# Performance work log

Measured on AMD Instinct MI355X. Metric: run time of the kernel, lower is better.

The kernel has to match this reference:

```python
import jax, jax.numpy as jnp
import numpy as np

N_NODES = 100000
N_EDGES = 1600000
B = 256
H = 512
HEADS = 8
DH = H // HEADS


def setup_inputs() -> dict:
    key = jax.random.key(0)
    ks = list(jax.random.split(key, 24))
    def nrm(i, shape, s=0.02):
        return jax.random.normal(ks[i], shape, jnp.float32) * s
    inp = {}
    inp["text_features"] = jax.random.normal(ks[0], (B, 768), jnp.float32)
    inp["video_features"] = jax.random.normal(ks[1], (B, 512), jnp.float32)
    inp["x"] = jax.random.normal(ks[2], (N_NODES, 64), jnp.float32)
    inp["edge_index"] = jax.random.randint(ks[3], (2, N_EDGES), 0, N_NODES, dtype=jnp.int32)
    # sorted node->graph assignment covering all B graphs (no empty segments)
    inp["batch_idx"] = ((jnp.arange(N_NODES) * B) // N_NODES).astype(jnp.int32)
    inp["Wt"] = nrm(4, (768, H)); inp["bt"] = jnp.zeros((H,), jnp.float32)
    inp["Wv"] = nrm(5, (512, H)); inp["bv"] = jnp.zeros((H,), jnp.float32)
    inp["Wq"] = nrm(6, (H, H)); inp["bq"] = jnp.zeros((H,), jnp.float32)
    inp["Wk"] = nrm(7, (H, H)); inp["bk"] = jnp.zeros((H,), jnp.float32)
    inp["Wva"] = nrm(8, (H, H)); inp["bva"] = jnp.zeros((H,), jnp.float32)
    inp["Wo"] = nrm(9, (H, H)); inp["bo"] = jnp.zeros((H,), jnp.float32)
    inp["Wf"] = nrm(10, (2 * H, H)); inp["bf"] = jnp.zeros((H,), jnp.float32)
    inp["G1W"] = nrm(11, (64, 128)); inp["G1b"] = jnp.zeros((128,), jnp.float32)
    inp["G2W"] = nrm(12, (128, 128)); inp["G2b"] = jnp.zeros((128,), jnp.float32)
    inp["G3W"] = nrm(13, (128, 256)); inp["G3b"] = jnp.zeros((256,), jnp.float32)
    inp["Wff"] = nrm(14, (H + 256, H)); inp["bff"] = jnp.zeros((H,), jnp.float32)
    inp["Wb"] = nrm(15, (H, 2)); inp["bb"] = jnp.zeros((2,), jnp.float32)
    inp["Wa"] = nrm(16, (H, 2)); inp["ba"] = jnp.zeros((2,), jnp.float32)
    return inp


def _gcn_conv(h, W, b, src, dst, dis):
    # PyG GCNConv: linear transform, symmetric-normalized aggregation w/ self-loops, bias
    hw = h @ W                                       # [N, C]
    norm = dis[src] * dis[dst]                       # [E]
    msg = hw[src] * norm[:, None]                    # [E, C]
    agg = jax.ops.segment_sum(msg, dst, num_segments=h.shape[0])
    agg = agg + hw * (dis * dis)[:, None]            # self-loop messages
    return agg + b


def reference(text_features, video_features, x, edge_index, batch_idx, Wt, bt, Wv, bv, Wq, bq, Wk, bk, Wva, bva, Wo, bo, Wf, bf, G1W, G1b, G2W, G2b, G3W, G3b, Wff, bff, Wb, bb, Wa, ba):
    # encoders (dropout is eval-mode no-op)
    text_enc = jax.nn.relu(text_features @ Wt + bt)      # [B, H]
    video_enc = jax.nn.relu(video_features @ Wv + bv)    # [B, H]
    # multihead attention; torch seq lens are both 1 (batch acts as N)
    q = (text_enc @ Wq + bq).reshape(B, HEADS, 1, DH)
    k = (video_enc @ Wk + bk).reshape(B, HEADS, 1, DH)
    v = (video_enc @ Wva + bva).reshape(B, HEADS, 1, DH)
    scores = jnp.einsum('bhqd,bhkd->bhqk', q, k) / np.float32(np.sqrt(DH))
    w = jax.nn.softmax(scores, axis=-1)
    attn = jnp.einsum('bhqk,bhkd->bhqd', w, v).reshape(B, H)
    text_attended = attn @ Wo + bo
    # multimodal fusion
    fused = jax.nn.relu(jnp.concatenate([text_attended, video_enc], axis=1) @ Wf + bf)
    # GCN stack
    src, dst = edge_index[0], edge_index[1]
    deg = jax.ops.segment_sum(jnp.ones((N_EDGES,), jnp.float32), dst, num_segments=N_NODES) + 1.0
    dis = jax.lax.rsqrt(deg)
    h = jax.nn.elu(_gcn_conv(x, G1W, G1b, src, dst, dis))
    h = jax.nn.elu(_gcn_conv(h, G2W, G2b, src, dst, dis))
    h = _gcn_conv(h, G3W, G3b, src, dst, dis)            # [N, 256]
    # per-graph mean pooling (the original per-batch Python loop, as one segment-mean)
    counts = jax.ops.segment_sum(jnp.ones((N_NODES,), jnp.float32), batch_idx, num_segments=B)
    pooled = jax.ops.segment_sum(h, batch_idx, num_segments=B) / counts[:, None]  # [B, 256]
    # final fusion + classifier heads
    final = jax.nn.relu(jnp.concatenate([fused, pooled], axis=1) @ Wff + bff)
    bullying = jax.nn.log_softmax(final @ Wb + bb, axis=1)
    aggression = jax.nn.log_softmax(final @ Wa + ba, axis=1)
    return bullying, aggression
```

## Files before the change

kernel.cpp:

```cpp
#include <hip/hip_runtime.h>
#include <hip/hip_bf16.h>

#define N_NODES 100000
#define NPAD    100096
#define N_EDGES 1600000
#define BATCH   256
#define HDIM    512

typedef unsigned short u16;
typedef __attribute__((ext_vector_type(8))) short bf16x8;
typedef __attribute__((ext_vector_type(8))) unsigned short u16x8;
typedef __attribute__((ext_vector_type(4))) float f32x4;

__device__ __forceinline__ float bf2f(u16 u) {
    union { unsigned i; float f; } v; v.i = ((unsigned)u) << 16; return v.f;
}
__device__ __forceinline__ u16 f2bf(float f) {
    __hip_bfloat16 h = __float2bfloat16(f);
    return *reinterpret_cast<u16*>(&h);
}

template<int K, int ACT, int SCALE>
__global__ __launch_bounds__(256) void gemm_mfma(
        const u16* __restrict__ A, const u16* __restrict__ Wt,
        const float* __restrict__ bias, const float* __restrict__ dis,
        u16* __restrict__ C, int N) {
    constexpr int RB = K * 2;
    __shared__ u16 As[128 * K];
    __shared__ u16 Bs[128 * K];
    const int tid  = threadIdx.x;
    const int lane = tid & 63;
    const int w    = tid >> 6;
    const int wr   = w >> 1, wc = w & 1;
    const int row0 = blockIdx.y * 128;
    const int col0 = blockIdx.x * 128;

    constexpr int WB     = 128 * RB / 4;
    constexpr int PASSES = WB / 1024;
    const size_t Abase = (size_t)row0 * K;
    const size_t Bbase = (size_t)col0 * K;
    #pragma unroll
    for (int p = 0; p < PASSES; ++p) {
        int Lb  = w * WB + p * 1024;
        int L   = Lb + lane * 16;
        int row = L / RB;
        int cb  = L % RB;
        int scb = cb ^ ((row & 7) << 4);
        const u16* ga = A  + Abase + (size_t)row * K + (scb >> 1);
        const u16* gb = Wt + Bbase + (size_t)row * K + (scb >> 1);
        __builtin_amdgcn_global_load_lds((const __attribute__((address_space(1))) void*)ga,
            (__attribute__((address_space(3))) void*)&As[Lb >> 1], 16, 0, 0);
        __builtin_amdgcn_global_load_lds((const __attribute__((address_space(1))) void*)gb,
            (__attribute__((address_space(3))) void*)&Bs[Lb >> 1], 16, 0, 0);
    }
    asm volatile("s_waitcnt vmcnt(0)" ::: "memory");
    __syncthreads();

    const int rl = lane & 15;
    const int kg = lane >> 4;
    f32x4 acc[4][4] = {};
    #pragma unroll
    for (int s = 0; s < K / 32; ++s) {
        bf16x8 af[4], bg[4];
        #pragma unroll
        for (int m = 0; m < 4; ++m) {
            int row = wr * 64 + m * 16 + rl;
            int cb  = s * 64 + kg * 16;
            int scb = cb ^ ((row & 7) << 4);
            af[m] = *(const bf16x8*)&As[(row * RB + scb) >> 1];
        }
        #pragma unroll
        for (int n = 0; n < 4; ++n) {
            int row = wc * 64 + n * 16 + rl;
            int cb  = s * 64 + kg * 16;
            int scb = cb ^ ((row & 7) << 4);
            bg[n] = *(const bf16x8*)&Bs[(row * RB + scb) >> 1];
        }
        #pragma unroll
        for (int m = 0; m < 4; ++m)
            #pragma unroll
            for (int n = 0; n < 4; ++n)
                acc[m][n] = __builtin_amdgcn_mfma_f32_16x16x32_bf16(af[m], bg[n], acc[m][n], 0, 0, 0);
    }

    #pragma unroll
    for (int m = 0; m < 4; ++m) {
        #pragma unroll
        for (int r = 0; r < 4; ++r) {
            int grow = row0 + wr * 64 + m * 16 + kg * 4 + r;
            float ds = SCALE ? dis[grow] : 1.f;
            #pragma unroll
            for (int n = 0; n < 4; ++n) {
                int gcol = col0 + wc * 64 + n * 16 + rl;
                float v = acc[m][n][r] + bias[gcol];
                if (ACT == 2) v = v > 0.f ? v : expm1f(v);
                C[(size_t)grow * N + gcol] = f2bf(v * ds);
            }
        }
    }
}

template<int ACT>
__global__ __launch_bounds__(256) void gemm64(
        const u16* __restrict__ A, const u16* __restrict__ Wt,
        const float* __restrict__ bias, u16* __restrict__ C,
        int K, int lda, int ldc) {
    __shared__ u16 As[64 * 64];
    __shared__ u16 Bs[64 * 64];
    const int tid  = threadIdx.x;
    const int lane = tid & 63;
    const int w    = tid >> 6;
    const int wr   = w >> 1, wc = w & 1;
    const int row0 = blockIdx.y * 64;
    const int col0 = blockIdx.x * 64;
    const int rl = lane & 15;
    const int kg = lane >> 4;
    f32x4 acc[2][2] = {};

    for (int k0 = 0; k0 < K; k0 += 64) {
        #pragma unroll
        for (int p = 0; p < 2; ++p) {
            int Lb  = w * 2048 + p * 1024;
            int L   = Lb + lane * 16;
            int row = L >> 7;
            int cb  = L & 127;
            int scb = cb ^ ((row & 7) << 4);
            const u16* ga = A  + (size_t)(row0 + row) * lda + k0 + (scb >> 1);
            const u16* gb = Wt + (size_t)(col0 + row) * K   + k0 + (scb >> 1);
            __builtin_amdgcn_global_load_lds((const __attribute__((address_space(1))) void*)ga,
                (__attribute__((address_space(3))) void*)&As[Lb >> 1], 16, 0, 0);
            __builtin_amdgcn_global_load_lds((const __attribute__((address_space(1))) void*)gb,
                (__attribute__((address_space(3))) void*)&Bs[Lb >> 1], 16, 0, 0);
        }
        asm volatile("s_waitcnt vmcnt(0)" ::: "memory");
        __syncthreads();
        #pragma unroll
        for (int s = 0; s < 2; ++s) {
            bf16x8 af[2], bg[2];
            #pragma unroll
            for (int m = 0; m < 2; ++m) {
                int row = wr * 32 + m * 16 + rl;
                int cb  = s * 64 + kg * 16;
                int scb = cb ^ ((row & 7) << 4);
                af[m] = *(const bf16x8*)&As[(row * 128 + scb) >> 1];
            }
            #pragma unroll
            for (int n = 0; n < 2; ++n) {
                int row = wc * 32 + n * 16 + rl;
                int cb  = s * 64 + kg * 16;
                int scb = cb ^ ((row & 7) << 4);
                bg[n] = *(const bf16x8*)&Bs[(row * 128 + scb) >> 1];
            }
            #pragma unroll
            for (int m = 0; m < 2; ++m)
                #pragma unroll
                for (int n = 0; n < 2; ++n)
                    acc[m][n] = __builtin_amdgcn_mfma_f32_16x16x32_bf16(af[m], bg[n], acc[m][n], 0, 0, 0);
        }
        __syncthreads();
    }

    #pragma unroll
    for (int m = 0; m < 2; ++m) {
        #pragma unroll
        for (int r = 0; r < 4; ++r) {
            int grow = row0 + wr * 32 + m * 16 + kg * 4 + r;
            #pragma unroll
            for (int n = 0; n < 2; ++n) {
                int gcol = col0 + wc * 32 + n * 16 + rl;
                float v = acc[m][n][r] + bias[gcol];
                if (ACT == 1) v = fmaxf(v, 0.f);
                C[(size_t)grow * ldc + gcol] = f2bf(v);
            }
        }
    }
}

template<int K, int N>
__device__ __forceinline__ void tw(const float* __restrict__ W, u16* __restrict__ Wt, int t) {
    int n = t / K, k = t - n * K;
    Wt[t] = f2bf(W[(size_t)k * N + n]);
}

#define DEG_BLKS 6250

__global__ void prep_deg(const int* __restrict__ dstE, int* __restrict__ deg,
                         int* __restrict__ slot,
                         const float* __restrict__ G1W, u16* __restrict__ g1wt,
                         const float* __restrict__ G2W, u16* __restrict__ g2wt,
                         const float* __restrict__ Wv,  u16* __restrict__ WvT,
                         const float* __restrict__ Wva, u16* __restrict__ WvaT,
                         const float* __restrict__ Wo,  u16* __restrict__ WoT,
                         const float* __restrict__ Wf,  u16* __restrict__ WfT,
                         const float* __restrict__ video, u16* __restrict__ vidbf) {
    int bid = blockIdx.x;
    const int tid = threadIdx.x;
    if (bid < DEG_BLKS) {
        int e = bid * 256 + tid;
        slot[e] = atomicAdd(&deg[dstE[e]], 1);
        return;
    }
    bid -= DEG_BLKS;
    if (bid < 32)        { tw<64, 128>  (G1W, g1wt, bid * 256 + tid); }
    else if (bid < 96)   { tw<128, 128> (G2W, g2wt, (bid - 32) * 256 + tid); }
    else if (bid < 1120) { tw<512, 512> (Wv,  WvT,  (bid - 96) * 256 + tid); }
    else if (bid < 2144) { tw<512, 512> (Wva, WvaT, (bid - 1120) * 256 + tid); }
    else if (bid < 3168) { tw<512, 512> (Wo,  WoT,  (bid - 2144) * 256 + tid); }
    else if (bid < 5216) { tw<1024, 512>(Wf,  WfT,  (bid - 3168) * 256 + tid); }
    else { int t = (bid - 5216) * 256 + tid; vidbf[t] = f2bf(video[t]); }
}

__global__ void final_fused(const u16* __restrict__ fusedb,
                            const float* __restrict__ pooled, const float* __restrict__ counts,
                            const float* __restrict__ G3W, const float* __restrict__ G3b,
                            const float* __restrict__ Wff, const float* __restrict__ bff,
                            const float* __restrict__ Wb,  const float* __restrict__ bb,
                            const float* __restrict__ Wa,  const float* __restrict__ ba,
                            float* __restrict__ out) {
    __shared__ float cat[768], fin[512], pp[128];
    __shared__ float rd[4][4];
    const int b = blockIdx.x, tid = threadIdx.x;
    cat[tid] = bf2f(fusedb[b * 512 + tid]);
    cat[tid + 256] = bf2f(fusedb[b * 512 + 256 + tid]);
    float inv = 1.f / counts[b];
    if (tid < 128) pp[tid] = pooled[b * 128 + tid] * inv;
    __syncthreads();
    {
        float s = G3b[tid];
        #pragma unroll 8
        for (int k = 0; k < 128; ++k) s += pp[k] * G3W[k * 256 + tid];
        cat[512 + tid] = s;
    }
    __syncthreads();
    {
        float a0 = bff[tid], a1 = bff[tid + 256];
        #pragma unroll 8
        for (int k = 0; k < 768; ++k) {
            float xv = cat[k];
            a0 += xv * Wff[k * 512 + tid];
            a1 += xv * Wff[k * 512 + tid + 256];
        }
        fin[tid] = fmaxf(a0, 0.f);
        fin[tid + 256] = fmaxf(a1, 0.f);
    }
    __syncthreads();
    float z0 = 0.f, z1 = 0.f, y0 = 0.f, y1 = 0.f;
    for (int k = tid; k < 512; k += 256) {
        float f = fin[k];
        z0 += f * Wb[2 * k];
        z1 += f * Wb[2 * k + 1];
        y0 += f * Wa[2 * k];
        y1 += f * Wa[2 * k + 1];
    }
    #pragma unroll
    for (int off = 32; off > 0; off >>= 1) {
        z0 += __shfl_down(z0, off);
        z1 += __shfl_down(z1, off);
        y0 += __shfl_down(y0, off);
        y1 += __shfl_down(y1, off);
    }
    int ww = tid >> 6;
    if ((tid & 63) == 0) { rd[ww][0] = z0; rd[ww][1] = z1; rd[ww][2] = y0; rd[ww][3] = y1; }
    __syncthreads();
    if (tid == 0) {
        float Z0 = rd[0][0] + rd[1][0] + rd[2][0] + rd[3][0] + bb[0];
        float Z1 = rd[0][1] + rd[1][1] + rd[2][1] + rd[3][1] + bb[1];
        float Y0 = rd[0][2] + rd[1][2] + rd[2][2] + rd[3][2] + ba[0];
        float Y1 = rd[0][3] + rd[1][3] + rd[2][3] + rd[3][3] + ba[1];
        float m = fmaxf(Z0, Z1);
        float l = m + logf(expf(Z0 - m) + expf(Z1 - m));
        out[b * 2 + 0] = Z0 - l;
        out[b * 2 + 1] = Z1 - l;
        float m2 = fmaxf(Y0, Y1);
        float l2 = m2 + logf(expf(Y0 - m2) + expf(Y1 - m2));
        out[512 + b * 2 + 0] = Y0 - l2;
        out[512 + b * 2 + 1] = Y1 - l2;
    }
}

__global__ void scan1(const int* __restrict__ in, int* __restrict__ out,
                      int* __restrict__ bsum, float* __restrict__ dis, int n) {
    __shared__ int ts[256];
    const int tid = threadIdx.x;
    const int base = blockIdx.x * 1024;
    int v[4];
    #pragma unroll
    for (int i = 0; i < 4; ++i) {
        int idx = base + tid * 4 + i;
        v[i] = (idx < n) ? in[idx] : 0;
        if (idx < NPAD) dis[idx] = rsqrtf((float)v[i] + 1.f);
    }
    ts[tid] = v[0] + v[1] + v[2] + v[3];
    __syncthreads();
    for (int off = 1; off < 256; off <<= 1) {
        int val = (tid >= off) ? ts[tid - off] : 0;
        __syncthreads();
        ts[tid] += val;
        __syncthreads();
    }
    int run = (tid == 0) ? 0 : ts[tid - 1];
    if (tid == 255) bsum[blockIdx.x] = ts[255];
    #pragma unroll
    for (int i = 0; i < 4; ++i) {
        int idx = base + tid * 4 + i;
        if (idx < n) out[idx] = run;
        run += v[i];
    }
}

__global__ void scan2(int* __restrict__ bsum, int nb) {
    int l = threadIdx.x;
    int a = (l < nb) ? bsum[l] : 0;
    int b = (l + 64 < nb) ? bsum[l + 64] : 0;
    int oa = a, ob = b;
    #pragma unroll
    for (int off = 1; off < 64; off <<= 1) {
        int t = __shfl_up(a, off);
        if (l >= off) a += t;
    }
    int totA = __shfl(a, 63);
    #pragma unroll
    for (int off = 1; off < 64; off <<= 1) {
        int t = __shfl_up(b, off);
        if (l >= off) b += t;
    }
    if (l < nb) bsum[l] = a - oa;
    if (l + 64 < nb) bsum[l + 64] = totA + b - ob;
}

__global__ void csr_scatter3(const int* __restrict__ srcE, const int* __restrict__ dstE,
                             const int* __restrict__ partial, const int* __restrict__ bsum,
                             const int* __restrict__ slot,
                             int* __restrict__ csr_src, int* __restrict__ rowptr) {
    int e = blockIdx.x * blockDim.x + threadIdx.x;
    if (e <= N_NODES) rowptr[e] = (e < N_NODES) ? (partial[e] + bsum[e >> 10]) : N_EDGES;
    if (e < N_EDGES) {
        int d = dstE[e];
        csr_src[partial[d] + bsum[d >> 10] + slot[e]] = srcE[e];
    }
}

__global__ void scale_rows64_bf16(const float* __restrict__ x, const float* __restrict__ dis,
                                  u16* __restrict__ out) {
    int t = blockIdx.x * blockDim.x + threadIdx.x;
    if (t >= N_NODES * 64) return;
    out[t] = f2bf(x[t] * dis[t >> 6]);
}

template<int C>
__global__ void csr_agg_bf16(const u16* __restrict__ Hs, const int* __restrict__ rowptr,
                             const int* __restrict__ csr_src, const float* __restrict__ dis,
                             u16* __restrict__ out) {
    constexpr int LPG = C / 8;
    constexpr int G   = 64 / LPG;
    int node = blockIdx.x * 4 + (threadIdx.x >> 6);
    if (node >= N_NODES) return;
    int lane = threadIdx.x & 63;
    int g  = lane / LPG;
    int cl = lane % LPG;
    int s0 = rowptr[node], s1 = rowptr[node + 1];
    float a[8] = {};
    if (g == 0) {
        u16x8 v = *(const u16x8*)&Hs[(size_t)node * C + cl * 8];
        #pragma unroll
        for (int j = 0; j < 8; ++j) a[j] = bf2f(v[j]);
    }
    int e = s0 + g;
    while (e + 3 * G < s1) {
        int sA = csr_src[e], sB = csr_src[e + G];
        int sC = csr_src[e + 2 * G], sD = csr_src[e + 3 * G];
        u16x8 vA = *(const u16x8*)&Hs[(size_t)sA * C + cl * 8];
        u16x8 vB = *(const u16x8*)&Hs[(size_t)sB * C + cl * 8];
        u16x8 vC = *(const u16x8*)&Hs[(size_t)sC * C + cl * 8];
        u16x8 vD = *(const u16x8*)&Hs[(size_t)sD * C + cl * 8];
        #pragma unroll
        for (int j = 0; j < 8; ++j)
            a[j] += (bf2f(vA[j]) + bf2f(vB[j])) + (bf2f(vC[j]) + bf2f(vD[j]));
        e += 4 * G;
    }
    while (e < s1) {
        int s = csr_src[e];
        u16x8 v = *(const u16x8*)&Hs[(size_t)s * C + cl * 8];
        #pragma unroll
        for (int j = 0; j < 8; ++j) a[j] += bf2f(v[j]);
        e += G;
    }
    #pragma unroll
    for (int m = LPG; m < 64; m <<= 1)
        #pragma unroll
        for (int j = 0; j < 8; ++j) a[j] += __shfl_xor(a[j], m);
    if (g == 0) {
        float dd = dis[node];
        u16x8 o;
        #pragma unroll
        for (int j = 0; j < 8; ++j) o[j] = f2bf(a[j] * dd);
        *(u16x8*)&out[(size_t)node * C + cl * 8] = o;
    }
}

__global__ __launch_bounds__(256) void csr_agg_pool(
        const u16* __restrict__ Hs, const int* __restrict__ rowptr,
        const int* __restrict__ csr_src, const float* __restrict__ dis,
        const int* __restrict__ batch,
        float* __restrict__ pooled, float* __restrict__ counts) {
    __shared__ float bins[2][128];
    __shared__ int cnt[2];
    const int tid = threadIdx.x;
    const int base = blockIdx.x * 16;
    if (tid < 128) { bins[0][tid] = 0.f; bins[1][tid] = 0.f; }
    if (tid < 2) cnt[tid] = 0;
    __syncthreads();
    const int lane = tid & 63;
    const int w = tid >> 6;
    const int g = lane >> 4;
    const int cl = lane & 15;
    const int b0 = batch[base];
    #pragma unroll
    for (int i = 0; i < 4; ++i) {
        const int node = base + w * 4 + i;
        const int s0 = rowptr[node], s1 = rowptr[node + 1];
        float a[8] = {};
        if (g == 0) {
            u16x8 v = *(const u16x8*)&Hs[(size_t)node * 128 + cl * 8];
            #pragma unroll
            for (int j = 0; j < 8; ++j) a[j] = bf2f(v[j]);
        }
        int e = s0 + g;
        while (e + 12 < s1) {
            int sA = csr_src[e], sB = csr_src[e + 4];
            int sC = csr_src[e + 8], sD = csr_src[e + 12];
            u16x8 vA = *(const u16x8*)&Hs[(size_t)sA * 128 + cl * 8];
            u16x8 vB = *(const u16x8*)&Hs[(size_t)sB * 128 + cl * 8];
            u16x8 vC = *(const u16x8*)&Hs[(size_t)sC * 128 + cl * 8];
            u16x8 vD = *(const u16x8*)&Hs[(size_t)sD * 128 + cl * 8];
            #pragma unroll
            for (int j = 0; j < 8; ++j)
                a[j] += (bf2f(vA[j]) + bf2f(vB[j])) + (bf2f(vC[j]) + bf2f(vD[j]));
            e += 16;
        }
        while (e < s1) {
            int s = csr_src[e];
            u16x8 v = *(const u16x8*)&Hs[(size_t)s * 128 + cl * 8];
            #pragma unroll
            for (int j = 0; j < 8; ++j) a[j] += bf2f(v[j]);
            e += 4;
        }
        #pragma unroll
        for (int m = 16; m < 64; m <<= 1)
            #pragma unroll
            for (int j = 0; j < 8; ++j) a[j] += __shfl_xor(a[j], m);
        if (g == 0) {
            int bin = (batch[node] != b0) ? 1 : 0;
            float dd = dis[node];
            #pragma unroll
            for (int j = 0; j < 8; ++j) atomicAdd(&bins[bin][cl * 8 + j], a[j] * dd);
            if (cl == 0) atomicAdd(&cnt[bin], 1);
        }
    }
    __syncthreads();
    int bin = tid >> 7, c = tid & 127;
    if (cnt[bin] > 0) atomicAdd(&pooled[(b0 + bin) * 128 + c], bins[bin][c]);
    if (tid < 2 && cnt[tid] > 0) atomicAdd(&counts[b0 + tid], (float)cnt[tid]);
}

extern "C" void kernel_launch(void* const* d_in, const int* in_sizes, int n_in,
                              void* d_out, int out_size, void* d_ws, size_t ws_size,
                              hipStream_t stream) {
    const float* video = (const float*)d_in[1];
    const float* x     = (const float*)d_in[2];
    const int*   eidx  = (const int*)d_in[3];
    const int*   batch = (const int*)d_in[4];
    const float* Wv  = (const float*)d_in[7],  *bv  = (const float*)d_in[8];
    const float* Wva = (const float*)d_in[13], *bva = (const float*)d_in[14];
    const float* Wo  = (const float*)d_in[15], *bo  = (const float*)d_in[16];
    const float* Wf  = (const float*)d_in[17], *bf  = (const float*)d_in[18];
    const float* G1W = (const float*)d_in[19], *G1b = (const float*)d_in[20];
    const float* G2W = (const float*)d_in[21], *G2b = (const float*)d_in[22];
    const float* G3W = (const float*)d_in[23], *G3b = (const float*)d_in[24];
    const float* Wff = (const float*)d_in[25], *bff = (const float*)d_in[26];
    const float* Wb  = (const float*)d_in[27], *bb  = (const float*)d_in[28];
    const float* Wa  = (const float*)d_in[29], *ba  = (const float*)d_in[30];
    const int* srcE = eidx;
    const int* dstE = eidx + N_EDGES;

    char* wsc = (char*)d_ws;
    size_t off = 0;
    auto alloc = [&](size_t bytes) { char* p = wsc + off; off += (bytes + 255) & ~(size_t)255; return p; };
    u16*   bufA    = (u16*)  alloc((size_t)NPAD * 128 * 2);
    u16*   bufB    = (u16*)  alloc((size_t)NPAD * 128 * 2);
    float* dis     = (float*)alloc(NPAD * 4);
    int*   deg     = (int*)  alloc(NPAD * 4);
    int*   partial = (int*)  alloc(N_NODES * 4);
    int*   rowptr  = (int*)  alloc((N_NODES + 1) * 4);
    int*   slot    = (int*)  alloc((size_t)N_EDGES * 4);
    int*   csrsrc  = (int*)  alloc((size_t)N_EDGES * 4);
    int*   bsum    = (int*)  alloc(128 * 4);
    u16*   g1wt    = (u16*)  alloc(128 * 64 * 2);
    u16*   g2wt    = (u16*)  alloc(128 * 128 * 2);
    u16*   WvT     = (u16*)  alloc(512 * 512 * 2);
    u16*   WvaT    = (u16*)  alloc(512 * 512 * 2);
    u16*   WoT     = (u16*)  alloc(512 * 512 * 2);
    u16*   WfT     = (u16*)  alloc(512 * 1024 * 2);
    u16*   vidbf   = (u16*)  alloc(BATCH * 512 * 2);
    u16*   catb    = (u16*)  alloc(BATCH * 1024 * 2);
    u16*   vattnb  = (u16*)  alloc(BATCH * 512 * 2);
    u16*   fusedb  = (u16*)  alloc(BATCH * 512 * 2);
    float* pooled  = (float*)alloc((BATCH * 128 + BATCH) * 4);
    float* counts  = pooled + BATCH * 128;

    const int NB = (N_NODES + 1023) / 1024;

    hipMemsetAsync(deg, 0, NPAD * 4, stream);
    hipMemsetAsync(pooled, 0, (BATCH * 128 + BATCH) * 4, stream);
    prep_deg<<<DEG_BLKS + 5728, 256, 0, stream>>>(dstE, deg, slot,
        G1W, g1wt, G2W, g2wt, Wv, WvT, Wva, WvaT, Wo, WoT, Wf, WfT, video, vidbf);

    scan1<<<NB, 256, 0, stream>>>(deg, partial, bsum, dis, N_NODES);
    scan2<<<1, 64, 0, stream>>>(bsum, NB);
    csr_scatter3<<<(N_EDGES + 255) / 256, 256, 0, stream>>>(srcE, dstE, partial, bsum,
                                                            slot, csrsrc, rowptr);

    dim3 fe512(8, 4);
    gemm64<1><<<fe512, 256, 0, stream>>>(vidbf, WvT, bv, catb + 512, 512, 512, 1024);
    gemm64<0><<<fe512, 256, 0, stream>>>(catb + 512, WvaT, bva, vattnb, 512, 1024, 512);
    gemm64<0><<<fe512, 256, 0, stream>>>(vattnb, WoT, bo, catb, 512, 512, 1024);
    gemm64<1><<<fe512, 256, 0, stream>>>(catb, WfT, bf, fusedb, 1024, 1024, 512);

    scale_rows64_bf16<<<(N_NODES * 64 + 255) / 256, 256, 0, stream>>>(x, dis, bufA);
    csr_agg_bf16<64><<<(N_NODES + 3) / 4, 256, 0, stream>>>(bufA, rowptr, csrsrc, dis, bufB);
    gemm_mfma<64, 2, 1><<<dim3(1, NPAD / 128), 256, 0, stream>>>(bufB, g1wt, G1b, dis, bufA, 128);
    csr_agg_bf16<128><<<(N_NODES + 3) / 4, 256, 0, stream>>>(bufA, rowptr, csrsrc, dis, bufB);
    gemm_mfma<128, 2, 1><<<dim3(1, NPAD / 128), 256, 0, stream>>>(bufB, g2wt, G2b, dis, bufA, 128);
    csr_agg_pool<<<N_NODES / 16, 256, 0, stream>>>(bufA, rowptr, csrsrc, dis, batch, pooled, counts);

    final_fused<<<BATCH, 256, 0, stream>>>(fusedb, pooled, counts, G3W, G3b,
                                           Wff, bff, Wb, bb, Wa, ba, (float*)d_out);
}
```

Baseline: 448.0 us.

## Store GCN hidden features in fp8 for gather aggregation; fuse scatter with scaling

The two 128-wide GEMM outputs are now written as fp8 e4m3 instead of bf16. The two aggregation kernels that follow gather these fp8 rows, which halves the bytes per random neighbor read in the memory-bound edge gathers. The CSR scatter and the x-scaling kernel are merged into one launch, and the two memsets are combined into one by making the pooled buffer contiguous with deg. The risk is accuracy: e4m3 keeps only 3 mantissa bits for the hidden activations, which may exceed tolerance.

Measured after the change: 434.1 us. -3.1%, faster.

```diff
diff --git a/kernel.cpp b/kernel.cpp
--- a/kernel.cpp
+++ b/kernel.cpp
@@ -1,5 +1,6 @@
 #include <hip/hip_runtime.h>
 #include <hip/hip_bf16.h>
+#include <hip/hip_fp8.h>
 
 #define N_NODES 100000
 #define NPAD    100096
@@ -8,8 +9,10 @@
 #define HDIM    512
 
 typedef unsigned short u16;
+typedef unsigned char  u8;
 typedef __attribute__((ext_vector_type(8))) short bf16x8;
 typedef __attribute__((ext_vector_type(8))) unsigned short u16x8;
+typedef __attribute__((ext_vector_type(8))) unsigned char u8x8;
 typedef __attribute__((ext_vector_type(4))) float f32x4;
 
 __device__ __forceinline__ float bf2f(u16 u) {
@@ -19,12 +22,18 @@
     __hip_bfloat16 h = __float2bfloat16(f);
     return *reinterpret_cast<u16*>(&h);
 }
-
-template<int K, int ACT, int SCALE>
+__device__ __forceinline__ u8 f2fp8(float f) {
+    __hip_fp8_e4m3 q(f); return (u8)q.__x;
+}
+__device__ __forceinline__ float fp82f(u8 b) {
+    __hip_fp8_e4m3 q; q.__x = (__hip_fp8_storage_t)b; return (float)q;
+}
+
+template<int K, int ACT, int SCALE, int F8>
 __global__ __launch_bounds__(256) void gemm_mfma(
         const u16* __restrict__ A, const u16* __restrict__ Wt,
         const float* __restrict__ bias, const float* __restrict__ dis,
-        u16* __restrict__ C, int N) {
+        void* __restrict__ Cv, int N) {
     constexpr int RB = K * 2;
     __shared__ u16 As[128 * K];
     __shared__ u16 Bs[128 * K];
@@ -94,7 +103,9 @@
                 int gcol = col0 + wc * 64 + n * 16 + rl;
                 float v = acc[m][n][r] + bias[gcol];
                 if (ACT == 2) v = v > 0.f ? v : expm1f(v);
-                C[(size_t)grow * N + gcol] = f2bf(v * ds);
+                v *= ds;
+                if (F8) ((u8*)Cv)[(size_t)grow * N + gcol] = f2fp8(v);
+                else    ((u16*)Cv)[(size_t)grow * N + gcol] = f2bf(v);
             }
         }
     }
@@ -328,65 +339,63 @@
     if (l + 64 < nb) bsum[l + 64] = totA + b - ob;
 }
 
-__global__ void csr_scatter3(const int* __restrict__ srcE, const int* __restrict__ dstE,
-                             const int* __restrict__ partial, const int* __restrict__ bsum,
-                             const int* __restrict__ slot,
-                             int* __restrict__ csr_src, int* __restrict__ rowptr) {
-    int e = blockIdx.x * blockDim.x + threadIdx.x;
-    if (e <= N_NODES) rowptr[e] = (e < N_NODES) ? (partial[e] + bsum[e >> 10]) : N_EDGES;
-    if (e < N_EDGES) {
+#define SCAT_BLKS 6250
+#define SCALE_BLKS 25000
+__global__ void scatter_scale(const int* __restrict__ srcE, const int* __restrict__ dstE,
+                              const int* __restrict__ partial, const int* __restrict__ bsum,
+                              const int* __restrict__ slot,
+                              int* __restrict__ csr_src, int* __restrict__ rowptr,
+                              const float* __restrict__ x, const float* __restrict__ dis,
+                              u16* __restrict__ hs0) {
+    const int bid = blockIdx.x, tid = threadIdx.x;
+    if (bid < SCAT_BLKS) {
+        int e = bid * 256 + tid;
+        if (e <= N_NODES) rowptr[e] = (e < N_NODES) ? (partial[e] + bsum[e >> 10]) : N_EDGES;
         int d = dstE[e];
         csr_src[partial[d] + bsum[d >> 10] + slot[e]] = srcE[e];
-    }
-}
-
-__global__ void scale_rows64_bf16(const float* __restrict__ x, const float* __restrict__ dis,
-                                  u16* __restrict__ out) {
-    int t = blockIdx.x * blockDim.x + threadIdx.x;
-    if (t >= N_NODES * 64) return;
-    out[t] = f2bf(x[t] * dis[t >> 6]);
-}
-
-template<int C>
-__global__ void csr_agg_bf16(const u16* __restrict__ Hs, const int* __restrict__ rowptr,
-                             const int* __restrict__ csr_src, const float* __restrict__ dis,
-                             u16* __restrict__ out) {
-    constexpr int LPG = C / 8;
-    constexpr int G   = 64 / LPG;
+        return;
+    }
+    int t = (bid - SCAT_BLKS) * 256 + tid;
+    hs0[t] = f2bf(x[t] * dis[t >> 6]);
+}
+
+__global__ void csr_agg64(const u16* __restrict__ Hs, const int* __restrict__ rowptr,
+                          const int* __restrict__ csr_src, const float* __restrict__ dis,
+                          u16* __restrict__ out) {
     int node = blockIdx.x * 4 + (threadIdx.x >> 6);
     if (node >= N_NODES) return;
     int lane = threadIdx.x & 63;
-    int g  = lane / LPG;
-    int cl = lane % LPG;
+    int g  = lane >> 3;
+    int cl = lane & 7;
     int s0 = rowptr[node], s1 = rowptr[node + 1];
     float a[8] = {};
     if (g == 0) {
-        u16x8 v = *(const u16x8*)&Hs[(size_t)node * C + cl * 8];
+        u16x8 v = *(const u16x8*)&Hs[(size_t)node * 64 + cl * 8];
         #pragma unroll
         for (int j = 0; j < 8; ++j) a[j] = bf2f(v[j]);
     }
     int e = s0 + g;
-    while (e + 3 * G < s1) {
-        int sA = csr_src[e], sB = csr_src[e + G];
-        int sC = csr_src[e + 2 * G], sD = csr_src[e + 3 * G];
-        u16x8 vA = *(const u16x8*)&Hs[(size_t)sA * C + cl * 8];
-        u16x8 vB = *(const u16x8*)&Hs[(size_t)sB * C + cl * 8];
-        u16x8 vC = *(const u16x8*)&Hs[(size_t)sC * C + cl * 8];
-        u16x8 vD = *(const u16x8*)&Hs[(size_t)sD * C + cl * 8];
+    while (e + 24 < s1) {
+        int sA = csr_src[e], sB = csr_src[e + 8];
+        int sC = csr_src[e + 16], sD = csr_src[e + 24];
+        u16x8 vA = *(const u16x8*)&Hs[(size_t)sA * 64 + cl * 8];
+        u16x8 vB = *(const u16x8*)&Hs[(size_t)sB * 64 + cl * 8];
+        u16x8 vC = *(const u16x8*)&Hs[(size_t)sC * 64 + cl * 8];
+        u16x8 vD = *(const u16x8*)&Hs[(size_t)sD * 64 + cl * 8];
         #pragma unroll
         for (int j = 0; j < 8; ++j)
             a[j] += (bf2f(vA[j]) + bf2f(vB[j])) + (bf2f(vC[j]) + bf2f(vD[j]));
-        e += 4 * G;
+        e += 32;
     }
     while (e < s1) {
         int s = csr_src[e];
-        u16x8 v = *(const u16x8*)&Hs[(size_t)s * C + cl * 8];
+        u16x8 v = *(const u16x8*)&Hs[(size_t)s * 64 + cl * 8];
         #pragma unroll
         for (int j = 0; j < 8; ++j) a[j] += bf2f(v[j]);
-        e += G;
-    }
-    #pragma unroll
-    for (int m = LPG; m < 64; m <<= 1)
+        e += 8;
+    }
+    #pragma unroll
+    for (int m = 8; m < 64; m <<= 1)
         #pragma unroll
         for (int j = 0; j < 8; ++j) a[j] += __shfl_xor(a[j], m);
     if (g == 0) {
@@ -394,12 +403,60 @@
         u16x8 o;
         #pragma unroll
         for (int j = 0; j < 8; ++j) o[j] = f2bf(a[j] * dd);
-        *(u16x8*)&out[(size_t)node * C + cl * 8] = o;
+        *(u16x8*)&out[(size_t)node * 64 + cl * 8] = o;
+    }
+}
+
+__global__ void csr_agg_fp8(const u8* __restrict__ Hs, const int* __restrict__ rowptr,
+                            const int* __restrict__ csr_src, const float* __restrict__ dis,
+                            u16* __restrict__ out) {
+    int node = blockIdx.x * 4 + (threadIdx.x >> 6);
+    if (node >= N_NODES) return;
+    int lane = threadIdx.x & 63;
+    int g  = lane >> 4;
+    int cl = lane & 15;
+    int s0 = rowptr[node], s1 = rowptr[node + 1];
+    float a[8] = {};
+    if (g == 0) {
+        u8x8 v = *(const u8x8*)&Hs[(size_t)node * 128 + cl * 8];
+        #pragma unroll
+        for (int j = 0; j < 8; ++j) a[j] = fp82f(v[j]);
+    }
+    int e = s0 + g;
+    while (e + 12 < s1) {
+        int sA = csr_src[e], sB = csr_src[e + 4];
+        int sC = csr_src[e + 8], sD = csr_src[e + 12];
+        u8x8 vA = *(const u8x8*)&Hs[(size_t)sA * 128 + cl * 8];
+        u8x8 vB = *(const u8x8*)&Hs[(size_t)sB * 128 + cl * 8];
+        u8x8 vC = *(const u8x8*)&Hs[(size_t)sC * 128 + cl * 8];
+        u8x8 vD = *(const u8x8*)&Hs[(size_t)sD * 128 + cl * 8];
+        #pragma unroll
+        for (int j = 0; j < 8; ++j)
+            a[j] += (fp82f(vA[j]) + fp82f(vB[j])) + (fp82f(vC[j]) + fp82f(vD[j]));
+        e += 16;
+    }
+    while (e < s1) {
+        int s = csr_src[e];
+        u8x8 v = *(const u8x8*)&Hs[(size_t)s * 128 + cl * 8];
+        #pragma unroll
+        for (int j = 0; j < 8; ++j) a[j] += fp82f(v[j]);
+        e += 4;
+    }
+    #pragma unroll
+    for (int m = 16; m < 64; m <<= 1)
+        #pragma unroll
+        for (int j = 0; j < 8; ++j) a[j] += __shfl_xor(a[j], m);
+    if (g == 0) {
+        float dd = dis[node];
+        u16x8 o;
+        #pragma unroll
+        for (int j = 0; j < 8; ++j) o[j] = f2bf(a[j] * dd);
+        *(u16x8*)&out[(size_t)node * 128 + cl * 8] = o;
     }
 }
 
 __global__ __launch_bounds__(256) void csr_agg_pool(
-        const u16* __restrict__ Hs, const int* __restrict__ rowptr,
+        const u8* __restrict__ Hs, const int* __restrict__ rowptr,
         const int* __restrict__ csr_src, const float* __restrict__ dis,
         const int* __restrict__ batch,
         float* __restrict__ pooled, float* __restrict__ counts) {
@@ -421,28 +478,28 @@
         const int s0 = rowptr[node], s1 = rowptr[node + 1];
         float a[8] = {};
         if (g == 0) {
-            u16x8 v = *(const u16x8*)&Hs[(size_t)node * 128 + cl * 8];
-            #pragma unroll
-            for (int j = 0; j < 8; ++j) a[j] = bf2f(v[j]);
+            u8x8 v = *(const u8x8*)&Hs[(size_t)node * 128 + cl * 8];
+            #pragma unroll
+            for (int j = 0; j < 8; ++j) a[j] = fp82f(v[j]);
         }
         int e = s0 + g;
         while (e + 12 < s1) {
             int sA = csr_src[e], sB = csr_src[e + 4];
             int sC = csr_src[e + 8], sD = csr_src[e + 12];
-            u16x8 vA = *(const u16x8*)&Hs[(size_t)sA * 128 + cl * 8];
-            u16x8 vB = *(const u16x8*)&Hs[(size_t)sB * 128 + cl * 8];
-            u16x8 vC = *(const u16x8*)&Hs[(size_t)sC * 128 + cl * 8];
-            u16x8 vD = *(const u16x8*)&Hs[(size_t)sD * 128 + cl * 8];
+            u8x8 vA = *(const u8x8*)&Hs[(size_t)sA * 128 + cl * 8];
+            u8x8 vB = *(const u8x8*)&Hs[(size_t)sB * 128 + cl * 8];
+            u8x8 vC = *(const u8x8*)&Hs[(size_t)sC * 128 + cl * 8];
+            u8x8 vD = *(const u8x8*)&Hs[(size_t)sD * 128 + cl * 8];
             #pragma unroll
             for (int j = 0; j < 8; ++j)
-                a[j] += (bf2f(vA[j]) + bf2f(vB[j])) + (bf2f(vC[j]) + bf2f(vD[j]));
+                a[j] += (fp82f(vA[j]) + fp82f(vB[j])) + (fp82f(vC[j]) + fp82f(vD[j]));
             e += 16;
         }
         while (e < s1) {
             int s = csr_src[e];
-            u16x8 v = *(const u16x8*)&Hs[(size_t)s * 128 + cl * 8];
-            #pragma unroll
-            for (int j = 0; j < 8; ++j) a[j] += bf2f(v[j]);
+            u8x8 v = *(const u8x8*)&Hs[(size_t)s * 128 + cl * 8];
+            #pragma unroll
+            for (int j = 0; j < 8; ++j) a[j] += fp82f(v[j]);
             e += 4;
         }
         #pragma unroll
@@ -490,6 +547,8 @@
     u16*   bufB    = (u16*)  alloc((size_t)NPAD * 128 * 2);
     float* dis     = (float*)alloc(NPAD * 4);
     int*   deg     = (int*)  alloc(NPAD * 4);
+    float* pooled  = (float*)alloc((BATCH * 128 + BATCH) * 4);
+    float* counts  = pooled + BATCH * 128;
     int*   partial = (int*)  alloc(N_NODES * 4);
     int*   rowptr  = (int*)  alloc((N_NODES + 1) * 4);
     int*   slot    = (int*)  alloc((size_t)N_EDGES * 4);
@@ -505,20 +564,18 @@
     u16*   catb    = (u16*)  alloc(BATCH * 1024 * 2);
     u16*   vattnb  = (u16*)  alloc(BATCH * 512 * 2);
     u16*   fusedb  = (u16*)  alloc(BATCH * 512 * 2);
-    float* pooled  = (float*)alloc((BATCH * 128 + BATCH) * 4);
-    float* counts  = pooled + BATCH * 128;
 
     const int NB = (N_NODES + 1023) / 1024;
 
-    hipMemsetAsync(deg, 0, NPAD * 4, stream);
-    hipMemsetAsync(pooled, 0, (BATCH * 128 + BATCH) * 4, stream);
+    hipMemsetAsync(deg, 0, NPAD * 4 + (BATCH * 128 + BATCH) * 4, stream);
+
     prep_deg<<<DEG_BLKS + 5728, 256, 0, stream>>>(dstE, deg, slot,
         G1W, g1wt, G2W, g2wt, Wv, WvT, Wva, WvaT, Wo, WoT, Wf, WfT, video, vidbf);
 
     scan1<<<NB, 256, 0, stream>>>(deg, partial, bsum, dis, N_NODES);
     scan2<<<1, 64, 0, stream>>>(bsum, NB);
-    csr_scatter3<<<(N_EDGES + 255) / 256, 256, 0, stream>>>(srcE, dstE, partial, bsum,
-                                                            slot, csrsrc, rowptr);
+    scatter_scale<<<SCAT_BLKS + SCALE_BLKS, 256, 0, stream>>>(
+        srcE, dstE, partial, bsum, slot, csrsrc, rowptr, x, dis, bufA);
 
     dim3 fe512(8, 4);
     gemm64<1><<<fe512, 256, 0, stream>>>(vidbf, WvT, bv, catb + 512, 512, 512, 1024);
@@ -526,12 +583,14 @@
     gemm64<0><<<fe512, 256, 0, stream>>>(vattnb, WoT, bo, catb, 512, 512, 1024);
     gemm64<1><<<fe512, 256, 0, stream>>>(catb, WfT, bf, fusedb, 1024, 1024, 512);
 
-    scale_rows64_bf16<<<(N_NODES * 64 + 255) / 256, 256, 0, stream>>>(x, dis, bufA);
-    csr_agg_bf16<64><<<(N_NODES + 3) / 4, 256, 0, stream>>>(bufA, rowptr, csrsrc, dis, bufB);
-    gemm_mfma<64, 2, 1><<<dim3(1, NPAD / 128), 256, 0, stream>>>(bufB, g1wt, G1b, dis, bufA, 128);
-    csr_agg_bf16<128><<<(N_NODES + 3) / 4, 256, 0, stream>>>(bufA, rowptr, csrsrc, dis, bufB);
-    gemm_mfma<128, 2, 1><<<dim3(1, NPAD / 128), 256, 0, stream>>>(bufB, g2wt, G2b, dis, bufA, 128);
-    csr_agg_pool<<<N_NODES / 16, 256, 0, stream>>>(bufA, rowptr, csrsrc, dis, batch, pooled, counts);
+    csr_agg64<<<(N_NODES + 3) / 4, 256, 0, stream>>>(bufA, rowptr, csrsrc, dis, bufB);
+    gemm_mfma<64, 2, 1, 1><<<dim3(1, NPAD / 128), 256, 0, stream>>>(
+        bufB, g1wt, G1b, dis, bufA, 128);
+    csr_agg_fp8<<<(N_NODES + 3) / 4, 256, 0, stream>>>((const u8*)bufA, rowptr, csrsrc, dis, bufB);
+    gemm_mfma<128, 2, 1, 1><<<dim3(1, NPAD / 128), 256, 0, stream>>>(
+        bufB, g2wt, G2b, dis, bufA, 128);
+    csr_agg_pool<<<N_NODES / 16, 256, 0, stream>>>((const u8*)bufA, rowptr, csrsrc, dis,
+                                                   batch, pooled, counts);
 
     final_fused<<<BATCH, 256, 0, stream>>>(fusedb, pooled, counts, G3W, G3b,
                                            Wff, bff, Wb, bb, Wa, ba, (float*)d_out);
```
